# Performance work log

Measured on AMD Instinct MI355X. Metric: run time of the kernel, lower is better.

## Reference

```python
import jax, jax.numpy as jnp
import numpy as np

N_NODES = 50000
N_EDGES = 800000
IN_CH = 128
HID = 128
NUM_GRAPHS = 512
BN_EPS = 1e-5


def setup_inputs() -> dict:
    key = jax.random.key(0)
    ks = jax.random.split(key, 16)
    x = jax.random.normal(ks[0], (N_NODES, IN_CH), dtype=jnp.float32)
    edge_index = jax.random.randint(ks[1], (2, N_EDGES), 0, N_NODES, dtype=jnp.int64)
    batch = jnp.sort(jax.random.randint(ks[2], (N_NODES,), 0, NUM_GRAPHS, dtype=jnp.int64))

    def glorot(k, shape):
        fan_in = shape[1]
        return jax.random.normal(k, shape, dtype=jnp.float32) / jnp.sqrt(jnp.float32(fan_in))

    # SAGEConv1: lin_l (aggr path, with bias), lin_r (root path, no bias)
    W1l = glorot(ks[3], (HID, IN_CH)); b1 = jnp.zeros((HID,), jnp.float32)
    W1r = glorot(ks[4], (HID, IN_CH))
    # SAGEConv2
    W2l = glorot(ks[5], (HID, HID)); b2 = jnp.zeros((HID,), jnp.float32)
    W2r = glorot(ks[6], (HID, HID))
    # MLP tail
    lin1_w = glorot(ks[7], (HID, HID)); lin1_b = jnp.zeros((HID,), jnp.float32)
    lin2_w = glorot(ks[8], (2, HID)); lin2_b = jnp.zeros((2,), jnp.float32)
    # BatchNorm1d (eval mode, running stats)
    gamma = jnp.ones((HID,), jnp.float32)
    beta = jnp.zeros((HID,), jnp.float32)
    running_mean = jax.random.normal(ks[9], (HID,), dtype=jnp.float32) * 0.1
    running_var = jax.random.uniform(ks[10], (HID,), dtype=jnp.float32, minval=0.5, maxval=1.5)
    return {
        "x": x, "edge_index": edge_index, "batch": batch,
        "W1l": W1l, "b1": b1, "W1r": W1r,
        "W2l": W2l, "b2": b2, "W2r": W2r,
        "lin1_w": lin1_w, "lin1_b": lin1_b,
        "lin2_w": lin2_w, "lin2_b": lin2_b,
        "gamma": gamma, "beta": beta,
        "running_mean": running_mean, "running_var": running_var,
    }


def _sage_conv(x, src, dst, Wl, bl, Wr):
    # mean-aggregate neighbor features (message flows src -> dst)
    n = x.shape[0]
    agg = jax.ops.segment_sum(x[src], dst, num_segments=n)  # [N, d]
    cnt = jax.ops.segment_sum(jnp.ones((src.shape[0], 1), x.dtype), dst, num_segments=n)
    mean = agg / jnp.maximum(cnt, 1.0)
    return mean @ Wl.T + bl + x @ Wr.T


def reference(x, edge_index, batch, W1l, b1, W1r, W2l, b2, W2r,
              lin1_w, lin1_b, lin2_w, lin2_b, gamma, beta,
              running_mean, running_var):
    src, dst = edge_index[0], edge_index[1]
    h = _sage_conv(x, src, dst, W1l, b1, W1r)      # [N, HID]
    h = _sage_conv(h, src, dst, W2l, b2, W2r)      # [N, HID]
    h = jax.ops.segment_sum(h, batch, num_segments=NUM_GRAPHS)  # global_add_pool -> [G, HID]
    h = h @ lin1_w.T + lin1_b
    # BatchNorm1d in eval mode (running stats)
    h = (h - running_mean) * jax.lax.rsqrt(running_var + BN_EPS) * gamma + beta
    h = jax.nn.relu(h)
    h = h @ lin2_w.T + lin2_b                      # [G, 2]
    # Dropout is identity in eval mode
    return h
```

## Files before the change

kernel.cpp:

```cpp
#include <hip/hip_runtime.h>
#include <hip/hip_bf16.h>

#define NN 50000
#define NE 800000
#define HID 128
#define NG 512
#define BN_EPS 1e-5f

typedef __attribute__((ext_vector_type(8))) short bf16x8;
typedef __attribute__((ext_vector_type(4))) float f32x4;

__device__ __forceinline__ ushort f2bf(float f) {
    uint u = __float_as_uint(f);
    uint r = (u + 0x7fffu + ((u >> 16) & 1u)) >> 16;
    return (ushort)r;
}
__device__ __forceinline__ float bf_lo(uint v) { return __uint_as_float(v << 16); }
__device__ __forceinline__ float bf_hi(uint v) { return __uint_as_float(v & 0xffff0000u); }

__global__ __launch_bounds__(256) void hist_kernel(const int* __restrict__ ei,
                                                   int E, int* __restrict__ deg,
                                                   int* __restrict__ rank) {
    int e = blockIdx.x * 256 + threadIdx.x;
    if (e >= E) return;
    int dst = ei[E + e];
    rank[e] = atomicAdd(&deg[dst], 1);
}

__global__ __launch_bounds__(256) void scan1_kernel(const int* __restrict__ deg,
                                                    int* __restrict__ row_start,
                                                    int* __restrict__ bsums, int n) {
    __shared__ int s[256];
    int i = blockIdx.x * 256 + threadIdx.x;
    int v = (i < n) ? deg[i] : 0;
    s[threadIdx.x] = v;
    __syncthreads();
    for (int off = 1; off < 256; off <<= 1) {
        int t = (threadIdx.x >= off) ? s[threadIdx.x - off] : 0;
        __syncthreads();
        s[threadIdx.x] += t;
        __syncthreads();
    }
    if (i < n) row_start[i] = s[threadIdx.x] - v;
    if (threadIdx.x == 255) bsums[blockIdx.x] = s[255];
}

__global__ __launch_bounds__(256) void scan2_kernel(int* __restrict__ bsums, int nb) {
    __shared__ int s[256];
    int v = (threadIdx.x < nb) ? bsums[threadIdx.x] : 0;
    s[threadIdx.x] = v;
    __syncthreads();
    for (int off = 1; off < 256; off <<= 1) {
        int t = (threadIdx.x >= off) ? s[threadIdx.x - off] : 0;
        __syncthreads();
        s[threadIdx.x] += t;
        __syncthreads();
    }
    if (threadIdx.x < nb) bsums[threadIdx.x] = s[threadIdx.x] - v;
}

__global__ __launch_bounds__(256) void scan3_kernel(int* __restrict__ row_start,
                                                    const int* __restrict__ bsums, int n) {
    int i = blockIdx.x * 256 + threadIdx.x;
    if (i < n) row_start[i] += bsums[blockIdx.x];
}

__global__ __launch_bounds__(256) void fill_kernel(const int* __restrict__ ei, int E,
                                                   const int* __restrict__ row_start,
                                                   const int* __restrict__ rank,
                                                   int* __restrict__ srclist) {
    int e = blockIdx.x * 256 + threadIdx.x;
    if (e >= E) return;
    int src = ei[e];
    int dst = ei[E + e];
    srclist[row_start[dst] + rank[e]] = src;
}

__global__ __launch_bounds__(256) void convert_bf16_kernel(const float* __restrict__ in,
                                                           ushort* __restrict__ out, int n4) {
    int i = blockIdx.x * 256 + threadIdx.x;
    if (i >= n4) return;
    float4 v = ((const float4*)in)[i];
    ushort4 o;
    o.x = f2bf(v.x);
    o.y = f2bf(v.y);
    o.z = f2bf(v.z);
    o.w = f2bf(v.w);
    ((ushort4*)out)[i] = o;
}

__global__ __launch_bounds__(64) void wprep_kernel(const float* __restrict__ W0,
                                                   const float* __restrict__ W1,
                                                   const float* __restrict__ W2,
                                                   const float* __restrict__ W3,
                                                   ushort* __restrict__ Wp) {
    int b = blockIdx.x;
    int m = b >> 5;
    int g = b & 31;
    int tile = g >> 2;
    int chunk = g & 3;
    int lane = threadIdx.x;
    const float* W = (m == 0) ? W0 : (m == 1) ? W1 : (m == 2) ? W2 : W3;
    int col = tile * 16 + (lane & 15);
    int k0 = chunk * 32 + (lane >> 4) * 8;
    ushort* dst = Wp + ((size_t)b * 64 + lane) * 8;
#pragma unroll
    for (int j = 0; j < 8; ++j) dst[j] = f2bf(W[col * HID + k0 + j]);
}

__global__ __launch_bounds__(256) void aggregate_kernel(const ushort* __restrict__ feat,
                                                        const int* __restrict__ row_start,
                                                        const int* __restrict__ deg,
                                                        const int* __restrict__ srclist,
                                                        ushort* __restrict__ mean, int n) {
    int node = blockIdx.x * 4 + (threadIdx.x >> 6);
    if (node >= n) return;
    int lane = threadIdx.x & 63;
    int cl = lane & 15;
    int sub = lane >> 4;
    const uint4* fb = (const uint4*)feat;
    int s0 = row_start[node];
    int d = deg[node];

    float a[8];
#pragma unroll
    for (int i = 0; i < 8; ++i) a[i] = 0.f;

    int j = 0;
    for (; j + 8 <= d; j += 8) {
        int i0 = srclist[s0 + j + sub];
        int i1 = srclist[s0 + j + 4 + sub];
        uint4 v0 = fb[(size_t)i0 * 16 + cl];
        uint4 v1 = fb[(size_t)i1 * 16 + cl];
        a[0] += bf_lo(v0.x) + bf_lo(v1.x);
        a[1] += bf_hi(v0.x) + bf_hi(v1.x);
        a[2] += bf_lo(v0.y) + bf_lo(v1.y);
        a[3] += bf_hi(v0.y) + bf_hi(v1.y);
        a[4] += bf_lo(v0.z) + bf_lo(v1.z);
        a[5] += bf_hi(v0.z) + bf_hi(v1.z);
        a[6] += bf_lo(v0.w) + bf_lo(v1.w);
        a[7] += bf_hi(v0.w) + bf_hi(v1.w);
    }
    for (; j < d; j += 4) {
        int idx = j + sub;
        bool valid = idx < d;
        int safe = valid ? idx : (d - 1);
        int src = srclist[s0 + safe];
        uint4 v = fb[(size_t)src * 16 + cl];
        float s = valid ? 1.f : 0.f;
        a[0] += s * bf_lo(v.x);
        a[1] += s * bf_hi(v.x);
        a[2] += s * bf_lo(v.y);
        a[3] += s * bf_hi(v.y);
        a[4] += s * bf_lo(v.z);
        a[5] += s * bf_hi(v.z);
        a[6] += s * bf_lo(v.w);
        a[7] += s * bf_hi(v.w);
    }

#pragma unroll
    for (int i = 0; i < 8; ++i) {
        float v = a[i];
        v += __shfl_xor(v, 16);
        v += __shfl_xor(v, 32);
        a[i] = v;
    }

    if (sub == 0) {
        float inv = 1.0f / fmaxf((float)d, 1.0f);
        uint4 o;
        o.x = (uint)f2bf(a[0] * inv) | ((uint)f2bf(a[1] * inv) << 16);
        o.y = (uint)f2bf(a[2] * inv) | ((uint)f2bf(a[3] * inv) << 16);
        o.z = (uint)f2bf(a[4] * inv) | ((uint)f2bf(a[5] * inv) << 16);
        o.w = (uint)f2bf(a[6] * inv) | ((uint)f2bf(a[7] * inv) << 16);
        ((uint4*)mean)[(size_t)node * 16 + cl] = o;
    }
}

template <bool POOL>
__global__ __launch_bounds__(256) void sage_gemm_mfma(const ushort* __restrict__ Amean,
                                                      const ushort* __restrict__ Aroot,
                                                      const ushort* __restrict__ WpL,
                                                      const float* __restrict__ bias,
                                                      const int* __restrict__ batch,
                                                      void* __restrict__ outv, int nwaves) {
    int w = blockIdx.x * 4 + (threadIdx.x >> 6);
    if (w >= nwaves) return;
    int lane = threadIdx.x & 63;
    int mrow = lane & 15;
    int quad = lane >> 4;
    int r0 = w * 16;

    f32x4 acc[8];
#pragma unroll
    for (int t = 0; t < 8; ++t) acc[t] = (f32x4){0.f, 0.f, 0.f, 0.f};

    const ushort* arow_m = Amean + ((size_t)(r0 + mrow)) * HID + quad * 8;
    const ushort* arow_r = Aroot + ((size_t)(r0 + mrow)) * HID + quad * 8;

#pragma unroll
    for (int half = 0; half < 2; ++half) {
        const ushort* arow = half ? arow_r : arow_m;
        const ushort* wb = WpL + (size_t)half * 16384 + (size_t)lane * 8;
#pragma unroll
        for (int c = 0; c < 4; ++c) {
            bf16x8 a = *(const bf16x8*)(arow + c * 32);
#pragma unroll
            for (int t = 0; t < 8; ++t) {
                bf16x8 b = *(const bf16x8*)(wb + (size_t)(t * 4 + c) * 512);
                acc[t] = __builtin_amdgcn_mfma_f32_16x16x32_bf16(a, b, acc[t], 0, 0, 0);
            }
        }
    }

    if (POOL) {
        float* pooled = (float*)outv;
        int rbase = r0 + quad * 4;
        int g0 = batch[rbase + 0];
        int g1 = batch[rbase + 1];
        int g2 = batch[rbase + 2];
        int g3 = batch[rbase + 3];
#pragma unroll
        for (int t = 0; t < 8; ++t) {
            int col = t * 16 + mrow;
            float bv = bias[col];
            float v0 = acc[t][0] + bv;
            float v1 = acc[t][1] + bv;
            float v2 = acc[t][2] + bv;
            float v3 = acc[t][3] + bv;
            int cg = g0;
            float s = v0;
            if (g1 == cg) s += v1; else { atomicAdd(&pooled[(size_t)cg * HID + col], s); cg = g1; s = v1; }
            if (g2 == cg) s += v2; else { atomicAdd(&pooled[(size_t)cg * HID + col], s); cg = g2; s = v2; }
            if (g3 == cg) s += v3; else { atomicAdd(&pooled[(size_t)cg * HID + col], s); cg = g3; s = v3; }
            atomicAdd(&pooled[(size_t)cg * HID + col], s);
        }
    } else {
        ushort* out = (ushort*)outv;
#pragma unroll
        for (int t = 0; t < 8; ++t) {
            int col = t * 16 + mrow;
            float bv = bias[col];
#pragma unroll
            for (int r = 0; r < 4; ++r) {
                int row = r0 + quad * 4 + r;
                out[(size_t)row * HID + col] = f2bf(acc[t][r] + bv);
            }
        }
    }
}

__global__ __launch_bounds__(128) void tail_kernel(const float* __restrict__ pooled,
                                                   const float* __restrict__ lin1_w,
                                                   const float* __restrict__ lin1_b,
                                                   const float* __restrict__ lin2_w,
                                                   const float* __restrict__ lin2_b,
                                                   const float* __restrict__ gamma,
                                                   const float* __restrict__ beta,
                                                   const float* __restrict__ rmean,
                                                   const float* __restrict__ rvar,
                                                   float* __restrict__ out) {
    __shared__ float Wt[64 * 128];
    __shared__ float p[128];
    __shared__ float tbuf[128];
    int g = blockIdx.x;
    int c = threadIdx.x;
    p[c] = pooled[g * HID + c];
    float acc = lin1_b[c];
    int kk = c & 63;
    int chalf = c >> 6;
    for (int k0 = 0; k0 < 128; k0 += 64) {
        __syncthreads();
        for (int i = 0; i < 64; ++i) {
            int crow = i * 2 + chalf;
            float v = lin1_w[crow * HID + k0 + kk];
            Wt[kk * 128 + (crow ^ (kk & 31))] = v;
        }
        __syncthreads();
#pragma unroll
        for (int k = 0; k < 64; ++k) {
            acc += p[k0 + k] * Wt[k * 128 + (c ^ (k & 31))];
        }
    }
    float v = (acc - rmean[c]) * rsqrtf(rvar[c] + BN_EPS) * gamma[c] + beta[c];
    v = fmaxf(v, 0.f);
    tbuf[c] = v;
    __syncthreads();
    int j = c >> 6;
    int lane = c & 63;
    float partial = tbuf[lane] * lin2_w[j * HID + lane] +
                    tbuf[lane + 64] * lin2_w[j * HID + lane + 64];
    for (int off = 32; off > 0; off >>= 1) partial += __shfl_down(partial, off);
    if (lane == 0) out[g * 2 + j] = partial + lin2_b[j];
}

extern "C" void kernel_launch(void* const* d_in, const int* in_sizes, int n_in,
                              void* d_out, int out_size, void* d_ws, size_t ws_size,
                              hipStream_t stream) {
    const float* x = (const float*)d_in[0];
    const int* ei = (const int*)d_in[1];
    const int* batch = (const int*)d_in[2];
    const float* W1l = (const float*)d_in[3];
    const float* b1 = (const float*)d_in[4];
    const float* W1r = (const float*)d_in[5];
    const float* W2l = (const float*)d_in[6];
    const float* b2 = (const float*)d_in[7];
    const float* W2r = (const float*)d_in[8];
    const float* lin1_w = (const float*)d_in[9];
    const float* lin1_b = (const float*)d_in[10];
    const float* lin2_w = (const float*)d_in[11];
    const float* lin2_b = (const float*)d_in[12];
    const float* gamma = (const float*)d_in[13];
    const float* beta = (const float*)d_in[14];
    const float* rmean = (const float*)d_in[15];
    const float* rvar = (const float*)d_in[16];
    float* out = (float*)d_out;

    const int N = NN, E = NE;
    const int NWAVES = N / 16;

    char* p = (char*)d_ws;
    auto carve = [&](size_t bytes) {
        void* r = (void*)p;
        p += (bytes + 255) & ~(size_t)255;
        return r;
    };
    int* deg = (int*)carve((size_t)N * 4);
    int* row_start = (int*)carve((size_t)N * 4);
    int* bsums = (int*)carve(1024 * 4);
    int* rank = (int*)carve((size_t)E * 4);
    int* srclist = (int*)carve((size_t)E * 4);
    ushort* xb = (ushort*)carve((size_t)N * HID * 2);
    ushort* meanb = (ushort*)carve((size_t)N * HID * 2);
    ushort* h1 = (ushort*)carve((size_t)N * HID * 2);
    float* pooled = (float*)carve((size_t)NG * HID * 4);
    ushort* Wp = (ushort*)carve(4 * 32 * 64 * 8 * 2);

    hipMemsetAsync(deg, 0, (size_t)N * 4, stream);
    hipMemsetAsync(pooled, 0, (size_t)NG * HID * 4, stream);

    const int scanBlocks = (N + 255) / 256;
    hist_kernel<<<(E + 255) / 256, 256, 0, stream>>>(ei, E, deg, rank);
    scan1_kernel<<<scanBlocks, 256, 0, stream>>>(deg, row_start, bsums, N);
    scan2_kernel<<<1, 256, 0, stream>>>(bsums, scanBlocks);
    scan3_kernel<<<scanBlocks, 256, 0, stream>>>(row_start, bsums, N);
    fill_kernel<<<(E + 255) / 256, 256, 0, stream>>>(ei, E, row_start, rank, srclist);

    convert_bf16_kernel<<<(N * HID / 4 + 255) / 256, 256, 0, stream>>>(x, xb, N * HID / 4);
    wprep_kernel<<<128, 64, 0, stream>>>(W1l, W1r, W2l, W2r, Wp);

    aggregate_kernel<<<(N + 3) / 4, 256, 0, stream>>>(xb, row_start, deg, srclist, meanb, N);
    sage_gemm_mfma<false><<<(NWAVES + 3) / 4, 256, 0, stream>>>(meanb, xb, Wp, b1, nullptr, h1,
                                                                NWAVES);
    aggregate_kernel<<<(N + 3) / 4, 256, 0, stream>>>(h1, row_start, deg, srclist, meanb, N);
    sage_gemm_mfma<true><<<(NWAVES + 3) / 4, 256, 0, stream>>>(meanb, h1, Wp + 32768, b2, batch,
                                                               pooled, NWAVES);
    tail_kernel<<<NG, 128, 0, stream>>>(pooled, lin1_w, lin1_b, lin2_w, lin2_b,
                                        gamma, beta, rmean, rvar, out);
}
```

Baseline: 271.3 us.

## Fuse neighbor mean aggregation into SAGE MFMA GEMM and merge prep/scan kernels

```diff
diff --git a/kernel.cpp b/kernel.cpp
--- a/kernel.cpp
+++ b/kernel.cpp
@@ -45,24 +45,17 @@
     if (threadIdx.x == 255) bsums[blockIdx.x] = s[255];
 }
 
-__global__ __launch_bounds__(256) void scan2_kernel(int* __restrict__ bsums, int nb) {
-    __shared__ int s[256];
-    int v = (threadIdx.x < nb) ? bsums[threadIdx.x] : 0;
-    s[threadIdx.x] = v;
+__global__ __launch_bounds__(256) void scan23_kernel(int* __restrict__ row_start,
+                                                     const int* __restrict__ bsums, int n) {
+    __shared__ int sred[4];
+    int v = (threadIdx.x < blockIdx.x) ? bsums[threadIdx.x] : 0;
+#pragma unroll
+    for (int off = 32; off > 0; off >>= 1) v += __shfl_xor(v, off);
+    if ((threadIdx.x & 63) == 0) sred[threadIdx.x >> 6] = v;
     __syncthreads();
-    for (int off = 1; off < 256; off <<= 1) {
-        int t = (threadIdx.x >= off) ? s[threadIdx.x - off] : 0;
-        __syncthreads();
-        s[threadIdx.x] += t;
-        __syncthreads();
-    }
-    if (threadIdx.x < nb) bsums[threadIdx.x] = s[threadIdx.x] - v;
-}
-
-__global__ __launch_bounds__(256) void scan3_kernel(int* __restrict__ row_start,
-                                                    const int* __restrict__ bsums, int n) {
+    int total = sred[0] + sred[1] + sred[2] + sred[3];
     int i = blockIdx.x * 256 + threadIdx.x;
-    if (i < n) row_start[i] += bsums[blockIdx.x];
+    if (i < n) row_start[i] += total;
 }
 
 __global__ __launch_bounds__(256) void fill_kernel(const int* __restrict__ ei, int E,
@@ -76,140 +69,135 @@
     srclist[row_start[dst] + rank[e]] = src;
 }
 
-__global__ __launch_bounds__(256) void convert_bf16_kernel(const float* __restrict__ in,
-                                                           ushort* __restrict__ out, int n4) {
-    int i = blockIdx.x * 256 + threadIdx.x;
-    if (i >= n4) return;
-    float4 v = ((const float4*)in)[i];
-    ushort4 o;
-    o.x = f2bf(v.x);
-    o.y = f2bf(v.y);
-    o.z = f2bf(v.z);
-    o.w = f2bf(v.w);
-    ((ushort4*)out)[i] = o;
-}
-
-__global__ __launch_bounds__(64) void wprep_kernel(const float* __restrict__ W0,
+#define CONV_BLOCKS 6250
+__global__ __launch_bounds__(256) void prep_kernel(const float* __restrict__ x,
+                                                   ushort* __restrict__ xb,
+                                                   const float* __restrict__ W0,
                                                    const float* __restrict__ W1,
                                                    const float* __restrict__ W2,
                                                    const float* __restrict__ W3,
                                                    ushort* __restrict__ Wp) {
-    int b = blockIdx.x;
-    int m = b >> 5;
-    int g = b & 31;
-    int tile = g >> 2;
-    int chunk = g & 3;
-    int lane = threadIdx.x;
-    const float* W = (m == 0) ? W0 : (m == 1) ? W1 : (m == 2) ? W2 : W3;
-    int col = tile * 16 + (lane & 15);
-    int k0 = chunk * 32 + (lane >> 4) * 8;
-    ushort* dst = Wp + ((size_t)b * 64 + lane) * 8;
-#pragma unroll
-    for (int j = 0; j < 8; ++j) dst[j] = f2bf(W[col * HID + k0 + j]);
-}
-
-__global__ __launch_bounds__(256) void aggregate_kernel(const ushort* __restrict__ feat,
-                                                        const int* __restrict__ row_start,
-                                                        const int* __restrict__ deg,
-                                                        const int* __restrict__ srclist,
-                                                        ushort* __restrict__ mean, int n) {
-    int node = blockIdx.x * 4 + (threadIdx.x >> 6);
-    if (node >= n) return;
-    int lane = threadIdx.x & 63;
-    int cl = lane & 15;
-    int sub = lane >> 4;
-    const uint4* fb = (const uint4*)feat;
-    int s0 = row_start[node];
-    int d = deg[node];
-
-    float a[8];
-#pragma unroll
-    for (int i = 0; i < 8; ++i) a[i] = 0.f;
-
-    int j = 0;
-    for (; j + 8 <= d; j += 8) {
-        int i0 = srclist[s0 + j + sub];
-        int i1 = srclist[s0 + j + 4 + sub];
-        uint4 v0 = fb[(size_t)i0 * 16 + cl];
-        uint4 v1 = fb[(size_t)i1 * 16 + cl];
-        a[0] += bf_lo(v0.x) + bf_lo(v1.x);
-        a[1] += bf_hi(v0.x) + bf_hi(v1.x);
-        a[2] += bf_lo(v0.y) + bf_lo(v1.y);
-        a[3] += bf_hi(v0.y) + bf_hi(v1.y);
-        a[4] += bf_lo(v0.z) + bf_lo(v1.z);
-        a[5] += bf_hi(v0.z) + bf_hi(v1.z);
-        a[6] += bf_lo(v0.w) + bf_lo(v1.w);
-        a[7] += bf_hi(v0.w) + bf_hi(v1.w);
-    }
-    for (; j < d; j += 4) {
-        int idx = j + sub;
-        bool valid = idx < d;
-        int safe = valid ? idx : (d - 1);
-        int src = srclist[s0 + safe];
-        uint4 v = fb[(size_t)src * 16 + cl];
-        float s = valid ? 1.f : 0.f;
-        a[0] += s * bf_lo(v.x);
-        a[1] += s * bf_hi(v.x);
-        a[2] += s * bf_lo(v.y);
-        a[3] += s * bf_hi(v.y);
-        a[4] += s * bf_lo(v.z);
-        a[5] += s * bf_hi(v.z);
-        a[6] += s * bf_lo(v.w);
-        a[7] += s * bf_hi(v.w);
-    }
-
-#pragma unroll
-    for (int i = 0; i < 8; ++i) {
-        float v = a[i];
-        v += __shfl_xor(v, 16);
-        v += __shfl_xor(v, 32);
-        a[i] = v;
-    }
-
-    if (sub == 0) {
-        float inv = 1.0f / fmaxf((float)d, 1.0f);
-        uint4 o;
-        o.x = (uint)f2bf(a[0] * inv) | ((uint)f2bf(a[1] * inv) << 16);
-        o.y = (uint)f2bf(a[2] * inv) | ((uint)f2bf(a[3] * inv) << 16);
-        o.z = (uint)f2bf(a[4] * inv) | ((uint)f2bf(a[5] * inv) << 16);
-        o.w = (uint)f2bf(a[6] * inv) | ((uint)f2bf(a[7] * inv) << 16);
-        ((uint4*)mean)[(size_t)node * 16 + cl] = o;
+    if (blockIdx.x < CONV_BLOCKS) {
+        int i = blockIdx.x * 256 + threadIdx.x;
+        float4 v = ((const float4*)x)[i];
+        ushort4 o;
+        o.x = f2bf(v.x);
+        o.y = f2bf(v.y);
+        o.z = f2bf(v.z);
+        o.w = f2bf(v.w);
+        ((ushort4*)xb)[i] = o;
+    } else {
+        int b = (blockIdx.x - CONV_BLOCKS) * 4 + (threadIdx.x >> 6);
+        if (b >= 128) return;
+        int lane = threadIdx.x & 63;
+        int m = b >> 5;
+        int g = b & 31;
+        int tile = g >> 2;
+        int chunk = g & 3;
+        const float* W = (m == 0) ? W0 : (m == 1) ? W1 : (m == 2) ? W2 : W3;
+        int col = tile * 16 + (lane & 15);
+        int k0 = chunk * 32 + (lane >> 4) * 8;
+        ushort* dst = Wp + ((size_t)b * 64 + lane) * 8;
+#pragma unroll
+        for (int j = 0; j < 8; ++j) dst[j] = f2bf(W[col * HID + k0 + j]);
     }
 }
 
 template <bool POOL>
-__global__ __launch_bounds__(256) void sage_gemm_mfma(const ushort* __restrict__ Amean,
-                                                      const ushort* __restrict__ Aroot,
-                                                      const ushort* __restrict__ WpL,
-                                                      const float* __restrict__ bias,
-                                                      const int* __restrict__ batch,
-                                                      void* __restrict__ outv, int nwaves) {
+__global__ __launch_bounds__(256) void sage_layer(const ushort* __restrict__ feat,
+                                                  const int* __restrict__ row_start,
+                                                  const int* __restrict__ deg,
+                                                  const int* __restrict__ srclist,
+                                                  const ushort* __restrict__ WpL,
+                                                  const float* __restrict__ bias,
+                                                  const int* __restrict__ batch,
+                                                  void* __restrict__ outv, int nwaves) {
     int w = blockIdx.x * 4 + (threadIdx.x >> 6);
     if (w >= nwaves) return;
     int lane = threadIdx.x & 63;
     int mrow = lane & 15;
     int quad = lane >> 4;
     int r0 = w * 16;
+    int node = r0 + mrow;
+    int s0 = row_start[node];
+    int d = deg[node];
+    const uint4* fb = (const uint4*)feat;
+
+    float m[32];
+#pragma unroll
+    for (int i = 0; i < 32; ++i) m[i] = 0.f;
+
+    int j = 0;
+    for (; j + 2 <= d; j += 2) {
+        int i0 = srclist[s0 + j];
+        int i1 = srclist[s0 + j + 1];
+        uint4 v0[4], v1[4];
+#pragma unroll
+        for (int c = 0; c < 4; ++c) {
+            v0[c] = fb[(size_t)i0 * 16 + c * 4 + quad];
+            v1[c] = fb[(size_t)i1 * 16 + c * 4 + quad];
+        }
+#pragma unroll
+        for (int c = 0; c < 4; ++c) {
+            m[c * 8 + 0] += bf_lo(v0[c].x) + bf_lo(v1[c].x);
+            m[c * 8 + 1] += bf_hi(v0[c].x) + bf_hi(v1[c].x);
+            m[c * 8 + 2] += bf_lo(v0[c].y) + bf_lo(v1[c].y);
+            m[c * 8 + 3] += bf_hi(v0[c].y) + bf_hi(v1[c].y);
+            m[c * 8 + 4] += bf_lo(v0[c].z) + bf_lo(v1[c].z);
+            m[c * 8 + 5] += bf_hi(v0[c].z) + bf_hi(v1[c].z);
+            m[c * 8 + 6] += bf_lo(v0[c].w) + bf_lo(v1[c].w);
+            m[c * 8 + 7] += bf_hi(v0[c].w) + bf_hi(v1[c].w);
+        }
+    }
+    if (j < d) {
+        int i0 = srclist[s0 + j];
+        uint4 v0[4];
+#pragma unroll
+        for (int c = 0; c < 4; ++c) v0[c] = fb[(size_t)i0 * 16 + c * 4 + quad];
+#pragma unroll
+        for (int c = 0; c < 4; ++c) {
+            m[c * 8 + 0] += bf_lo(v0[c].x);
+            m[c * 8 + 1] += bf_hi(v0[c].x);
+            m[c * 8 + 2] += bf_lo(v0[c].y);
+            m[c * 8 + 3] += bf_hi(v0[c].y);
+            m[c * 8 + 4] += bf_lo(v0[c].z);
+            m[c * 8 + 5] += bf_hi(v0[c].z);
+            m[c * 8 + 6] += bf_lo(v0[c].w);
+            m[c * 8 + 7] += bf_hi(v0[c].w);
+        }
+    }
+
+    float inv = 1.0f / fmaxf((float)d, 1.0f);
+    bf16x8 amean[4];
+#pragma unroll
+    for (int c = 0; c < 4; ++c)
+#pragma unroll
+        for (int jj = 0; jj < 8; ++jj) amean[c][jj] = (short)f2bf(m[c * 8 + jj] * inv);
 
     f32x4 acc[8];
 #pragma unroll
     for (int t = 0; t < 8; ++t) acc[t] = (f32x4){0.f, 0.f, 0.f, 0.f};
 
-    const ushort* arow_m = Amean + ((size_t)(r0 + mrow)) * HID + quad * 8;
-    const ushort* arow_r = Aroot + ((size_t)(r0 + mrow)) * HID + quad * 8;
-
-#pragma unroll
-    for (int half = 0; half < 2; ++half) {
-        const ushort* arow = half ? arow_r : arow_m;
-        const ushort* wb = WpL + (size_t)half * 16384 + (size_t)lane * 8;
-#pragma unroll
-        for (int c = 0; c < 4; ++c) {
-            bf16x8 a = *(const bf16x8*)(arow + c * 32);
-#pragma unroll
-            for (int t = 0; t < 8; ++t) {
-                bf16x8 b = *(const bf16x8*)(wb + (size_t)(t * 4 + c) * 512);
-                acc[t] = __builtin_amdgcn_mfma_f32_16x16x32_bf16(a, b, acc[t], 0, 0, 0);
-            }
+    const ushort* arow_r = feat + (size_t)node * HID + quad * 8;
+    const ushort* wb0 = WpL + (size_t)lane * 8;
+    const ushort* wb1 = WpL + 16384 + (size_t)lane * 8;
+
+#pragma unroll
+    for (int c = 0; c < 4; ++c) {
+        bf16x8 a = amean[c];
+#pragma unroll
+        for (int t = 0; t < 8; ++t) {
+            bf16x8 b = *(const bf16x8*)(wb0 + (size_t)(t * 4 + c) * 512);
+            acc[t] = __builtin_amdgcn_mfma_f32_16x16x32_bf16(a, b, acc[t], 0, 0, 0);
+        }
+    }
+#pragma unroll
+    for (int c = 0; c < 4; ++c) {
+        bf16x8 a = *(const bf16x8*)(arow_r + c * 32);
+#pragma unroll
+        for (int t = 0; t < 8; ++t) {
+            bf16x8 b = *(const bf16x8*)(wb1 + (size_t)(t * 4 + c) * 512);
+            acc[t] = __builtin_amdgcn_mfma_f32_16x16x32_bf16(a, b, acc[t], 0, 0, 0);
         }
     }
 
@@ -331,7 +319,6 @@
     int* rank = (int*)carve((size_t)E * 4);
     int* srclist = (int*)carve((size_t)E * 4);
     ushort* xb = (ushort*)carve((size_t)N * HID * 2);
-    ushort* meanb = (ushort*)carve((size_t)N * HID * 2);
     ushort* h1 = (ushort*)carve((size_t)N * HID * 2);
     float* pooled = (float*)carve((size_t)NG * HID * 4);
     ushort* Wp = (ushort*)carve(4 * 32 * 64 * 8 * 2);
@@ -342,19 +329,15 @@
     const int scanBlocks = (N + 255) / 256;
     hist_kernel<<<(E + 255) / 256, 256, 0, stream>>>(ei, E, deg, rank);
     scan1_kernel<<<scanBlocks, 256, 0, stream>>>(deg, row_start, bsums, N);
-    scan2_kernel<<<1, 256, 0, stream>>>(bsums, scanBlocks);
-    scan3_kernel<<<scanBlocks, 256, 0, stream>>>(row_start, bsums, N);
+    scan23_kernel<<<scanBlocks, 256, 0, stream>>>(row_start, bsums, N);
     fill_kernel<<<(E + 255) / 256, 256, 0, stream>>>(ei, E, row_start, rank, srclist);
 
-    convert_bf16_kernel<<<(N * HID / 4 + 255) / 256, 256, 0, stream>>>(x, xb, N * HID / 4);
-    wprep_kernel<<<128, 64, 0, stream>>>(W1l, W1r, W2l, W2r, Wp);
-
-    aggregate_kernel<<<(N + 3) / 4, 256, 0, stream>>>(xb, row_start, deg, srclist, meanb, N);
-    sage_gemm_mfma<false><<<(NWAVES + 3) / 4, 256, 0, stream>>>(meanb, xb, Wp, b1, nullptr, h1,
-                                                                NWAVES);
-    aggregate_kernel<<<(N + 3) / 4, 256, 0, stream>>>(h1, row_start, deg, srclist, meanb, N);
-    sage_gemm_mfma<true><<<(NWAVES + 3) / 4, 256, 0, stream>>>(meanb, h1, Wp + 32768, b2, batch,
-                                                               pooled, NWAVES);
+    prep_kernel<<<CONV_BLOCKS + 32, 256, 0, stream>>>(x, xb, W1l, W1r, W2l, W2r, Wp);
+
+    sage_layer<false><<<(NWAVES + 3) / 4, 256, 0, stream>>>(xb, row_start, deg, srclist, Wp, b1,
+                                                            nullptr, h1, NWAVES);
+    sage_layer<true><<<(NWAVES + 3) / 4, 256, 0, stream>>>(h1, row_start, deg, srclist,
+                                                           Wp + 32768, b2, batch, pooled, NWAVES);
     tail_kernel<<<NG, 128, 0, stream>>>(pooled, lin1_w, lin1_b, lin2_w, lin2_b,
                                         gamma, beta, rmean, rvar, out);
 }
```

Result: slower. 295.1 us (+8.8%).
